# Kernel optimization log

Measured on AMD Instinct MI355X. Metric: run time of the kernel, lower is better.

Reference implementation:

```python
import jax, jax.numpy as jnp
import numpy as np
from jax import lax

B, L, H = 4096, 2048, 256


def setup_inputs() -> dict:
    key = jax.random.key(0)
    ks = jax.random.split(key, 7)
    s = 1.0 / np.sqrt(H)
    u = lambda k, shape: jax.random.uniform(k, shape, jnp.float32, -s, s)
    return {
        "x": jax.random.normal(ks[0], (B, L), jnp.float32),
        "W_ih": u(ks[1], (H, 1)),
        "b_ih": u(ks[2], (H,)),
        "W_hh": u(ks[3], (H, H)),
        "b_hh": u(ks[4], (H,)),
        "W_lin": u(ks[5], (1, H)),
        "b_lin": u(ks[6], (1,)),
        "future": 128,
    }


def reference(x, W_ih, b_ih, W_hh, b_hh, W_lin, b_lin, future):
    # RNNCell: h' = tanh(x_t W_ih^T + b_ih + h W_hh^T + b_hh); x_t is [B,1]
    def cell(inp, h):
        return jnp.tanh(inp @ W_ih.T + b_ih + h @ W_hh.T + b_hh)

    def lin(h):  # [B,H] -> [B]
        return (h @ W_lin.T + b_lin)[:, 0]

    def step(h, x_t):  # x_t: [B]
        h = cell(x_t[:, None], h)
        return h, lin(h)

    h0 = jnp.zeros((x.shape[0], W_hh.shape[0]), x.dtype)
    h, outs = lax.scan(step, h0, x.T)  # outs: [L, B]

    def fstep(carry, _):
        h, o = carry
        h = cell(o[:, None], h)
        o2 = lin(h)
        return (h, o2), o2

    (_, _), fouts = lax.scan(fstep, (h, outs[-1]), None, length=future)  # [future, B]
    return jnp.concatenate([outs, fouts], axis=0).T  # [B, L+future]
```

## Files before the change

### kernel.cpp

```cpp
#include <hip/hip_runtime.h>
#include <hip/hip_bf16.h>

typedef _Float16 half8 __attribute__((ext_vector_type(8)));
typedef _Float16 half4 __attribute__((ext_vector_type(4)));
typedef float    floatx4 __attribute__((ext_vector_type(4)));

#define B_TOT 4096
#define L_SEQ 2048
#define H_DIM 256
#define FUT   128
#define T_TOT (L_SEQ + FUT)
#define ROWS  16
#define CHUNK 256

__device__ __forceinline__ float tanh_fast(float p) {
    float e = __builtin_amdgcn_exp2f(p * 2.885390082f);
    return __builtin_fmaf(-2.0f, __builtin_amdgcn_rcpf(e + 1.0f), 1.0f);
}

__global__ __launch_bounds__(512, 2) void rnn_seq_kernel(
    const float* __restrict__ x,
    const float* __restrict__ W_ih,
    const float* __restrict__ b_ih,
    const float* __restrict__ W_hh,
    const float* __restrict__ b_hh,
    const float* __restrict__ W_lin,
    const float* __restrict__ b_lin,
    float* __restrict__ out)
{
    __shared__ __align__(16) unsigned char hbuf[2][ROWS * H_DIM * 2];
    __shared__ __align__(16) float xbuf[CHUNK * 17];
    __shared__ __align__(16) float obuf2[2][32][17];

    const int tid  = threadIdx.x;
    const int l    = tid & 63;
    const int w    = tid >> 6;
    const int ln15 = l & 15;
    const int lg   = l >> 4;
    const int b0   = blockIdx.x * ROWS;

    half8 wf[2][8];
    #pragma unroll
    for (int i = 0; i < 2; ++i) {
        const int n = (2 * w + i) * 16 + ln15;
        #pragma unroll
        for (int kk = 0; kk < 8; ++kk) {
            const float* p = W_hh + n * H_DIM + kk * 32 + lg * 8;
            half8 v;
            #pragma unroll
            for (int j = 0; j < 8; ++j) v[j] = (_Float16)p[j];
            wf[i][kk] = v;
        }
    }
    half8 wlf[8];
    #pragma unroll
    for (int kk = 0; kk < 8; ++kk) {
        const int kbase = kk * 32 + lg * 8;
        half8 v;
        #pragma unroll
        for (int j = 0; j < 8; ++j)
            v[j] = (ln15 == 0) ? (_Float16)W_lin[kbase + j] : (_Float16)0.0f;
        wlf[kk] = v;
    }
    floatx4 wih4[2], bia4[2];
    #pragma unroll
    for (int i = 0; i < 2; ++i) {
        const int n0 = (2 * w + i) * 16 + lg * 4;
        #pragma unroll
        for (int r = 0; r < 4; ++r) {
            wih4[i][r] = W_ih[n0 + r];
            bia4[i][r] = b_ih[n0 + r] + b_hh[n0 + r];
        }
    }
    const float blin = b_lin[0];
    float wl[8];
    #pragma unroll
    for (int j = 0; j < 8; ++j) wl[j] = W_lin[(tid & 31) * 8 + j];

    int aoff[8];
    #pragma unroll
    for (int kk = 0; kk < 8; ++kk)
        aoff[kk] = (ln15 * 512 + kk * 64 + lg * 16) ^ ((ln15 & 7) << 4);
    int woff2[2];
    #pragma unroll
    for (int i = 0; i < 2; ++i)
        woff2[i] = (ln15 * 512 + (2 * w + i) * 32 + lg * 8) ^ ((ln15 & 7) << 4);

    *(floatx4*)(hbuf[0] + tid * 16) = floatx4{0.f, 0.f, 0.f, 0.f};
    __syncthreads();

    int cur = 0;
    for (int s = 1; s <= T_TOT; ++s) {
        const int t_out = s - 2;

        if (t_out >= 32 && (t_out & 31) == 0) {
            const int tb = t_out - 32, par = (tb >> 5) & 1;
            const int row = tid >> 5, tt = tid & 31;
            out[(size_t)(b0 + row) * T_TOT + tb + tt] = obuf2[par][tt][row] + blin;
        }

        const bool fut = (s > L_SEQ);
        float xm = 0.0f;
        if (!fut) {
            if (((s - 1) & (CHUNK - 1)) == 0) {
                #pragma unroll
                for (int jj = 0; jj < 8; ++jj) {
                    const int idx = jj * 512 + tid;
                    const int row = idx >> 8, tl = idx & 255;
                    xbuf[tl * 17 + row] = x[(size_t)(b0 + row) * L_SEQ + (s - 1) + tl];
                }
                __syncthreads();
            }
            xm = xbuf[((s - 1) & (CHUNK - 1)) * 17 + ln15];
        }

        half8 a[8];
        #pragma unroll
        for (int kk = 0; kk < 8; ++kk)
            a[kk] = *(const half8*)(hbuf[cur] + aoff[kk]);

        floatx4 acc[2];
        #pragma unroll
        for (int i = 0; i < 2; ++i) {
            #pragma unroll
            for (int r = 0; r < 4; ++r)
                acc[i][r] = fut ? bia4[i][r]
                                : __builtin_fmaf(xm, wih4[i][r], bia4[i][r]);
        }
        #pragma unroll
        for (int kk = 0; kk < 8; ++kk) {
            acc[0] = __builtin_amdgcn_mfma_f32_16x16x32_f16(wf[0][kk], a[kk], acc[0], 0, 0, 0);
            acc[1] = __builtin_amdgcn_mfma_f32_16x16x32_f16(wf[1][kk], a[kk], acc[1], 0, 0, 0);
        }
        if (w == 0) {
            floatx4 al = floatx4{0, 0, 0, 0};
            #pragma unroll
            for (int kk = 0; kk < 8; ++kk)
                al = __builtin_amdgcn_mfma_f32_16x16x32_f16(wlf[kk], a[kk], al, 0, 0, 0);
            if (lg == 0 && s >= 2)
                obuf2[(t_out >> 5) & 1][t_out & 31][ln15] = al[0];
        }

        if (fut) {
            __syncthreads();
            xm = obuf2[(t_out >> 5) & 1][t_out & 31][ln15] + blin;
        }

        #pragma unroll
        for (int i = 0; i < 2; ++i) {
            half4 hv;
            #pragma unroll
            for (int r = 0; r < 4; ++r) {
                const float pre = fut ? __builtin_fmaf(xm, wih4[i][r], acc[i][r])
                                      : acc[i][r];
                hv[r] = (_Float16)tanh_fast(pre);
            }
            *(half4*)(hbuf[cur ^ 1] + woff2[i]) = hv;
        }
        __syncthreads();
        cur ^= 1;
    }

    {
        const int m = tid >> 5, kb = (tid & 31) * 8;
        const int off = (m * 512 + kb * 2) ^ ((m & 7) << 4);
        const half8 hv = *(const half8*)(hbuf[cur] + off);
        float dot = 0.f;
        #pragma unroll
        for (int j = 0; j < 8; ++j) dot += (float)hv[j] * wl[j];
        #pragma unroll
        for (int msk = 1; msk < 32; msk <<= 1) dot += __shfl_xor(dot, msk, 32);
        if ((tid & 31) == 0) obuf2[1][31][m] = dot;
    }
    __syncthreads();
    {
        const int row = tid >> 5, tt = tid & 31;
        out[(size_t)(b0 + row) * T_TOT + 2144 + tt] = obuf2[1][tt][row] + blin;
    }
}

extern "C" void kernel_launch(void* const* d_in, const int* in_sizes, int n_in,
                              void* d_out, int out_size, void* d_ws, size_t ws_size,
                              hipStream_t stream) {
    const float* x     = (const float*)d_in[0];
    const float* W_ih  = (const float*)d_in[1];
    const float* b_ih  = (const float*)d_in[2];
    const float* W_hh  = (const float*)d_in[3];
    const float* b_hh  = (const float*)d_in[4];
    const float* W_lin = (const float*)d_in[5];
    const float* b_lin = (const float*)d_in[6];
    float* out = (float*)d_out;
    rnn_seq_kernel<<<B_TOT / ROWS, 512, 0, stream>>>(x, W_ih, b_ih, W_hh, b_hh, W_lin, b_lin, out);
}
```

Before: 1.713 ms.

## Halve block to four waves with four MFMA tiles each, split loop phases

Each block now runs 256 threads, and each wave owns four 16-row tiles of W_hh kept in registers, so every wave issues more MFMAs per recurrent step and fewer waves meet at each barrier. The time loop is split into a sequence phase and a future phase, which removes per-step branches on the fut flag. The x staging chunk is halved, and the final output projection now reuses the MFMA path. The cost is roughly double the weight registers per thread and one block per CU at launch bounds (256,1), which reduces latency hiding and occupancy.

New measurement: 1.864 ms. 8.8% more time.

```diff
diff --git a/kernel.cpp b/kernel.cpp
--- a/kernel.cpp
+++ b/kernel.cpp
@@ -11,14 +11,14 @@
 #define FUT   128
 #define T_TOT (L_SEQ + FUT)
 #define ROWS  16
-#define CHUNK 256
+#define CHUNK 128
 
 __device__ __forceinline__ float tanh_fast(float p) {
     float e = __builtin_amdgcn_exp2f(p * 2.885390082f);
     return __builtin_fmaf(-2.0f, __builtin_amdgcn_rcpf(e + 1.0f), 1.0f);
 }
 
-__global__ __launch_bounds__(512, 2) void rnn_seq_kernel(
+__global__ __launch_bounds__(256, 1) void rnn_seq_kernel(
     const float* __restrict__ x,
     const float* __restrict__ W_ih,
     const float* __restrict__ b_ih,
@@ -39,10 +39,10 @@
     const int lg   = l >> 4;
     const int b0   = blockIdx.x * ROWS;
 
-    half8 wf[2][8];
-    #pragma unroll
-    for (int i = 0; i < 2; ++i) {
-        const int n = (2 * w + i) * 16 + ln15;
+    half8 wf[4][8];
+    #pragma unroll
+    for (int i = 0; i < 4; ++i) {
+        const int n = (4 * w + i) * 16 + ln15;
         #pragma unroll
         for (int kk = 0; kk < 8; ++kk) {
             const float* p = W_hh + n * H_DIM + kk * 32 + lg * 8;
@@ -62,10 +62,10 @@
             v[j] = (ln15 == 0) ? (_Float16)W_lin[kbase + j] : (_Float16)0.0f;
         wlf[kk] = v;
     }
-    floatx4 wih4[2], bia4[2];
-    #pragma unroll
-    for (int i = 0; i < 2; ++i) {
-        const int n0 = (2 * w + i) * 16 + lg * 4;
+    floatx4 wih4[4], bia4[4];
+    #pragma unroll
+    for (int i = 0; i < 4; ++i) {
+        const int n0 = (4 * w + i) * 16 + lg * 4;
         #pragma unroll
         for (int r = 0; r < 4; ++r) {
             wih4[i][r] = W_ih[n0 + r];
@@ -73,64 +73,60 @@
         }
     }
     const float blin = b_lin[0];
-    float wl[8];
-    #pragma unroll
-    for (int j = 0; j < 8; ++j) wl[j] = W_lin[(tid & 31) * 8 + j];
 
     int aoff[8];
     #pragma unroll
     for (int kk = 0; kk < 8; ++kk)
         aoff[kk] = (ln15 * 512 + kk * 64 + lg * 16) ^ ((ln15 & 7) << 4);
-    int woff2[2];
-    #pragma unroll
-    for (int i = 0; i < 2; ++i)
-        woff2[i] = (ln15 * 512 + (2 * w + i) * 32 + lg * 8) ^ ((ln15 & 7) << 4);
-
-    *(floatx4*)(hbuf[0] + tid * 16) = floatx4{0.f, 0.f, 0.f, 0.f};
+    int woff4[4];
+    #pragma unroll
+    for (int i = 0; i < 4; ++i)
+        woff4[i] = (ln15 * 512 + (4 * w + i) * 32 + lg * 8) ^ ((ln15 & 7) << 4);
+
+    *(floatx4*)(hbuf[0] + tid * 32)      = floatx4{0.f, 0.f, 0.f, 0.f};
+    *(floatx4*)(hbuf[0] + tid * 32 + 16) = floatx4{0.f, 0.f, 0.f, 0.f};
     __syncthreads();
 
     int cur = 0;
-    for (int s = 1; s <= T_TOT; ++s) {
+
+    for (int s = 1; s <= L_SEQ; ++s) {
         const int t_out = s - 2;
-
         if (t_out >= 32 && (t_out & 31) == 0) {
             const int tb = t_out - 32, par = (tb >> 5) & 1;
-            const int row = tid >> 5, tt = tid & 31;
-            out[(size_t)(b0 + row) * T_TOT + tb + tt] = obuf2[par][tt][row] + blin;
-        }
-
-        const bool fut = (s > L_SEQ);
-        float xm = 0.0f;
-        if (!fut) {
-            if (((s - 1) & (CHUNK - 1)) == 0) {
-                #pragma unroll
-                for (int jj = 0; jj < 8; ++jj) {
-                    const int idx = jj * 512 + tid;
-                    const int row = idx >> 8, tl = idx & 255;
-                    xbuf[tl * 17 + row] = x[(size_t)(b0 + row) * L_SEQ + (s - 1) + tl];
-                }
-                __syncthreads();
+            const int tt = tid & 31;
+            #pragma unroll
+            for (int jj = 0; jj < 2; ++jj) {
+                const int row = (tid >> 5) + 8 * jj;
+                out[(size_t)(b0 + row) * T_TOT + tb + tt] = obuf2[par][tt][row] + blin;
             }
-            xm = xbuf[((s - 1) & (CHUNK - 1)) * 17 + ln15];
-        }
+        }
+        if (((s - 1) & (CHUNK - 1)) == 0) {
+            #pragma unroll
+            for (int jj = 0; jj < 8; ++jj) {
+                const int idx = jj * 256 + tid;
+                const int row = idx >> 7, tl = idx & 127;
+                xbuf[tl * 17 + row] = x[(size_t)(b0 + row) * L_SEQ + (s - 1) + tl];
+            }
+            __syncthreads();
+        }
+        const float xm = xbuf[((s - 1) & (CHUNK - 1)) * 17 + ln15];
 
         half8 a[8];
         #pragma unroll
         for (int kk = 0; kk < 8; ++kk)
             a[kk] = *(const half8*)(hbuf[cur] + aoff[kk]);
 
-        floatx4 acc[2];
-        #pragma unroll
-        for (int i = 0; i < 2; ++i) {
+        floatx4 acc[4];
+        #pragma unroll
+        for (int i = 0; i < 4; ++i)
             #pragma unroll
             for (int r = 0; r < 4; ++r)
-                acc[i][r] = fut ? bia4[i][r]
-                                : __builtin_fmaf(xm, wih4[i][r], bia4[i][r]);
-        }
+                acc[i][r] = __builtin_fmaf(xm, wih4[i][r], bia4[i][r]);
         #pragma unroll
         for (int kk = 0; kk < 8; ++kk) {
-            acc[0] = __builtin_amdgcn_mfma_f32_16x16x32_f16(wf[0][kk], a[kk], acc[0], 0, 0, 0);
-            acc[1] = __builtin_amdgcn_mfma_f32_16x16x32_f16(wf[1][kk], a[kk], acc[1], 0, 0, 0);
+            #pragma unroll
+            for (int i = 0; i < 4; ++i)
+                acc[i] = __builtin_amdgcn_mfma_f32_16x16x32_f16(wf[i][kk], a[kk], acc[i], 0, 0, 0);
         }
         if (w == 0) {
             floatx4 al = floatx4{0, 0, 0, 0};
@@ -140,42 +136,84 @@
             if (lg == 0 && s >= 2)
                 obuf2[(t_out >> 5) & 1][t_out & 31][ln15] = al[0];
         }
-
-        if (fut) {
-            __syncthreads();
-            xm = obuf2[(t_out >> 5) & 1][t_out & 31][ln15] + blin;
-        }
-
-        #pragma unroll
-        for (int i = 0; i < 2; ++i) {
+        #pragma unroll
+        for (int i = 0; i < 4; ++i) {
             half4 hv;
             #pragma unroll
-            for (int r = 0; r < 4; ++r) {
-                const float pre = fut ? __builtin_fmaf(xm, wih4[i][r], acc[i][r])
-                                      : acc[i][r];
-                hv[r] = (_Float16)tanh_fast(pre);
-            }
-            *(half4*)(hbuf[cur ^ 1] + woff2[i]) = hv;
+            for (int r = 0; r < 4; ++r) hv[r] = (_Float16)tanh_fast(acc[i][r]);
+            *(half4*)(hbuf[cur ^ 1] + woff4[i]) = hv;
         }
         __syncthreads();
         cur ^= 1;
     }
 
-    {
-        const int m = tid >> 5, kb = (tid & 31) * 8;
-        const int off = (m * 512 + kb * 2) ^ ((m & 7) << 4);
-        const half8 hv = *(const half8*)(hbuf[cur] + off);
-        float dot = 0.f;
-        #pragma unroll
-        for (int j = 0; j < 8; ++j) dot += (float)hv[j] * wl[j];
-        #pragma unroll
-        for (int msk = 1; msk < 32; msk <<= 1) dot += __shfl_xor(dot, msk, 32);
-        if ((tid & 31) == 0) obuf2[1][31][m] = dot;
+    for (int s = L_SEQ + 1; s <= T_TOT; ++s) {
+        const int t_out = s - 2;
+        if ((t_out & 31) == 0) {
+            const int tb = t_out - 32, par = (tb >> 5) & 1;
+            const int tt = tid & 31;
+            #pragma unroll
+            for (int jj = 0; jj < 2; ++jj) {
+                const int row = (tid >> 5) + 8 * jj;
+                out[(size_t)(b0 + row) * T_TOT + tb + tt] = obuf2[par][tt][row] + blin;
+            }
+        }
+        half8 a[8];
+        #pragma unroll
+        for (int kk = 0; kk < 8; ++kk)
+            a[kk] = *(const half8*)(hbuf[cur] + aoff[kk]);
+
+        floatx4 al = floatx4{0, 0, 0, 0};
+        if (w == 0) {
+            #pragma unroll
+            for (int kk = 0; kk < 8; ++kk)
+                al = __builtin_amdgcn_mfma_f32_16x16x32_f16(wlf[kk], a[kk], al, 0, 0, 0);
+            if (lg == 0)
+                obuf2[(t_out >> 5) & 1][t_out & 31][ln15] = al[0];
+        }
+        floatx4 acc[4];
+        #pragma unroll
+        for (int i = 0; i < 4; ++i) acc[i] = bia4[i];
+        #pragma unroll
+        for (int kk = 0; kk < 8; ++kk) {
+            #pragma unroll
+            for (int i = 0; i < 4; ++i)
+                acc[i] = __builtin_amdgcn_mfma_f32_16x16x32_f16(wf[i][kk], a[kk], acc[i], 0, 0, 0);
+        }
+        __syncthreads();
+        const float xm = obuf2[(t_out >> 5) & 1][t_out & 31][ln15] + blin;
+
+        #pragma unroll
+        for (int i = 0; i < 4; ++i) {
+            half4 hv;
+            #pragma unroll
+            for (int r = 0; r < 4; ++r)
+                hv[r] = (_Float16)tanh_fast(__builtin_fmaf(xm, wih4[i][r], acc[i][r]));
+            *(half4*)(hbuf[cur ^ 1] + woff4[i]) = hv;
+        }
+        __syncthreads();
+        cur ^= 1;
+    }
+
+    if (w == 0) {
+        half8 a[8];
+        #pragma unroll
+        for (int kk = 0; kk < 8; ++kk)
+            a[kk] = *(const half8*)(hbuf[cur] + aoff[kk]);
+        floatx4 al = floatx4{0, 0, 0, 0};
+        #pragma unroll
+        for (int kk = 0; kk < 8; ++kk)
+            al = __builtin_amdgcn_mfma_f32_16x16x32_f16(wlf[kk], a[kk], al, 0, 0, 0);
+        if (lg == 0) obuf2[1][31][ln15] = al[0];
     }
     __syncthreads();
     {
-        const int row = tid >> 5, tt = tid & 31;
-        out[(size_t)(b0 + row) * T_TOT + 2144 + tt] = obuf2[1][tt][row] + blin;
+        const int tt = tid & 31;
+        #pragma unroll
+        for (int jj = 0; jj < 2; ++jj) {
+            const int row = (tid >> 5) + 8 * jj;
+            out[(size_t)(b0 + row) * T_TOT + 2144 + tt] = obuf2[1][tt][row] + blin;
+        }
     }
 }
 
@@ -190,5 +228,5 @@
     const float* W_lin = (const float*)d_in[5];
     const float* b_lin = (const float*)d_in[6];
     float* out = (float*)d_out;
-    rnn_seq_kernel<<<B_TOT / ROWS, 512, 0, stream>>>(x, W_ih, b_ih, W_hh, b_hh, W_lin, b_lin, out);
+    rnn_seq_kernel<<<B_TOT / ROWS, 256, 0, stream>>>(x, W_ih, b_ih, W_hh, b_hh, W_lin, b_lin, out);
 }
```
